# Kernel tuning notes

Measured on AMD Instinct MI355X. Metric: run time of the kernel, lower is better.

## Reference

```python
import jax, jax.numpy as jnp
import numpy as np

# photophysics rates from the original __init__
R_ISC, R_F, R_EXC, R_IC = 3e6, 5e7, 1e6, 7e7
R_ISC_S0, R_S1_OFF, R_OFF_S0 = 1e5, 2e4, 2.0e-1
RATE_MATRIX = np.array([
    [0.0,  R_EXC, 0.0,   0.0,      0.0],
    [R_F,  0.0,   R_ISC, R_S1_OFF, R_IC],
    [R_ISC_S0, 0.0, 0.0, 0.0,      0.0],
    [R_OFF_S0, 0.0, 0.0, 0.0,      0.0],
], dtype=np.float64)
ROW_SUMS = RATE_MATRIX.sum(axis=1)            # Exponential rates per state
CUM_PROBS = np.cumsum(RATE_MATRIX / ROW_SUMS[:, None], axis=1)  # (4,5) CDF rows
N_BINS = 200000      # torch.arange(0, 400, 0.002)
BIN_WIDTH = 0.002
STEPS, N_SAMPLE = 20000, 2048


def setup_inputs() -> dict:
    key = jax.random.key(0)
    k1, k2 = jax.random.split(key)
    u_cat = jax.random.uniform(k1, (STEPS, N_SAMPLE), dtype=jnp.float32)
    u_exp = jax.random.uniform(k2, (STEPS, N_SAMPLE), dtype=jnp.float32)
    return {"u_cat": u_cat, "u_exp": u_exp}


def reference(u_cat, u_exp):
    cum_probs = jnp.asarray(CUM_PROBS, dtype=jnp.float32)   # (4,5)
    row_rates = jnp.asarray(ROW_SUMS, dtype=jnp.float32)    # (4,)
    n_sample = u_cat.shape[1]

    def step(state, us):
        uc, ue = us                                  # (n,), (n,)
        cp = cum_probs[state]                        # (n,5) CDF of current state row
        # Categorical sample via inverse CDF: first bin whose cdf exceeds u
        t = jnp.argmax(uc[:, None] < cp, axis=-1)    # transition index 0..4
        photon = (t == 1)                            # photon_mat[1,0] == 1
        # Exponential dwell time in the *current* state (inverse CDF)
        dwell = -jnp.log1p(-ue) / row_rates[state]
        # transition_matrix maps t<4 -> state t, t==4 -> state 0
        new_state = jnp.where(t == 4, 0, t).astype(state.dtype)
        return new_state, (photon, dwell)

    state0 = jnp.zeros(n_sample, dtype=jnp.int32)    # all emitters start in S0
    _, (photons, dwells) = jax.lax.scan(step, state0, (u_cat, u_exp))

    cum_time = jnp.cumsum(dwells, axis=0)            # (steps, n_sample)
    bins = jnp.arange(N_BINS, dtype=jnp.float32) * BIN_WIDTH
    ind = jnp.searchsorted(bins, cum_time, side='left')  # torch.bucketize
    v = ind * photons.astype(ind.dtype)              # frame index per photon, 0 otherwise
    # on-device histogram replacing the CPU np.unique loop: counts of each v value
    hist = jnp.zeros(N_BINS + 1, dtype=jnp.int32).at[v.reshape(-1)].add(1)
    return photons.astype(jnp.float32), cum_time, hist
```

## Files before the change

### kernel.cpp

```cpp
#include <hip/hip_runtime.h>
#include <math.h>

#define STEPS  20000
#define NS     2048
#define NBINS  200000
#define SEGLEN 80
#define NSEG   250
#define NT     512000
#define NT4    128000
#define WPS    5

typedef float        f32x4 __attribute__((ext_vector_type(4)));
typedef unsigned int u32x4 __attribute__((ext_vector_type(4)));

constexpr double S1d = 5e7 + 3e6 + 2e4 + 7e7;
constexpr double P0d = 5e7 / S1d;
constexpr double P2d = 3e6 / S1d;
constexpr double P3d = 2e4 / S1d;
constexpr float C0 = (float)(P0d);
constexpr float C2 = (float)(P0d + P2d);
constexpr float C3 = (float)((P0d + P2d) + P3d);

constexpr float INV_R0 = 1.0f / 1e6f;
constexpr float INV_R1 = 1.0f / 123020000.0f;
constexpr float INV_R2 = 1.0f / 1e5f;
constexpr float INV_R3 = 5.0f;

#define WS_T1P   0u
#define WS_MAPS  10240000u
#define WS_PCNT4 10752000u
#define WS_SUMS4 12800000u
#define WS_ENTER 20992000u
#define WS_OFFS  21504000u
#define WS_PTOT  23552000u

__device__ __forceinline__ int te_decode(float u1) {
    return (u1 < C2) ? ((u1 < C0) ? 0 : 2) : ((u1 < C3) ? 3 : 0);
}
__device__ __forceinline__ int next_state(int s, int te) {
    return (s == 0) ? 1 : ((s == 1) ? te : 0);
}
__device__ __forceinline__ float inv_of(int s) {
    return (s == 0) ? INV_R0 : ((s == 1) ? INV_R1 : ((s == 2) ? INV_R2 : INV_R3));
}
__device__ __forceinline__ float dwell_base(float ue) {
    return -__logf(1.0f - ue);
}

__device__ __forceinline__ int bucketize(float v) {
    int lo = (int)(v * 500.0f) - 2;
    lo = lo < 0 ? 0 : lo;
#pragma unroll
    for (int i = 0; i < 4; ++i) lo += ((float)lo * 0.002f < v) ? 1 : 0;
    return lo > NBINS ? NBINS : lo;
}

__global__ void zero_kernel(float* __restrict__ hist, int* __restrict__ ptot) {
    int i = blockIdx.x * blockDim.x + threadIdx.x;
    if (i <= NBINS) hist[i] = 0.0f;
    if (i == 0) *ptot = 0;
}

__global__ void __launch_bounds__(256)
map_dwell_kernel(const float* __restrict__ u_cat, const float* __restrict__ u_exp,
                 unsigned int* __restrict__ t1p, unsigned char* __restrict__ maps,
                 unsigned int* __restrict__ pcnt4, float4* __restrict__ sums4)
{
    const int q = blockIdx.x * 256 + threadIdx.x;
    const int seg  = q >> 9;
    const int colq = q & 511;
    const int tbase = seg * NS + colq * 4;
    const size_t f4b = (size_t)seg * SEGLEN * (NS / 4) + colq;
    const f32x4* uc4 = (const f32x4*)u_cat + f4b;
    const f32x4* ue4 = (const f32x4*)u_exp + f4b;

    f32x4 uc[2][4], ue[2][4];
#pragma unroll
    for (int j = 0; j < 4; ++j) {
        uc[0][j] = __builtin_nontemporal_load(uc4 + (size_t)j * (NS / 4));
        ue[0][j] = ue4[(size_t)j * (NS / 4)];
    }
    int st[4][4], n[4][4];
    float s[4][4];
#pragma unroll
    for (int c = 0; c < 4; ++c)
#pragma unroll
        for (int e = 0; e < 4; ++e) { st[c][e] = e; n[c][e] = 0; s[c][e] = 0.0f; }
    unsigned int wc[4] = {0u, 0u, 0u, 0u};

#pragma unroll
    for (int ch = 0; ch < 20; ++ch) {
        const int cur = ch & 1, nxt = cur ^ 1;
        if (ch < 19) {
            const size_t rb = (size_t)(ch + 1) * 4 * (NS / 4);
#pragma unroll
            for (int j = 0; j < 4; ++j) {
                uc[nxt][j] = __builtin_nontemporal_load(uc4 + rb + (size_t)j * (NS / 4));
                ue[nxt][j] = ue4[rb + (size_t)j * (NS / 4)];
            }
        }
#pragma unroll
        for (int j = 0; j < 4; ++j) {
            const int sidx = ch * 4 + j;
#pragma unroll
            for (int c = 0; c < 4; ++c) {
                const int te = te_decode(uc[cur][j][c]);
                wc[c] |= (unsigned int)te << (2 * (sidx & 15));
                const float b = dwell_base(ue[cur][j][c]);
#pragma unroll
                for (int e = 0; e < 4; ++e) {
                    n[c][e] += (st[c][e] == 0);
                    s[c][e] += b * inv_of(st[c][e]);
                    st[c][e] = next_state(st[c][e], te);
                }
            }
        }
        if ((ch & 3) == 3) {
            u32x4 wv = {wc[0], wc[1], wc[2], wc[3]};
            *(u32x4*)(t1p + (size_t)(ch >> 2) * NT + tbase) = wv;
            wc[0] = wc[1] = wc[2] = wc[3] = 0u;
        }
    }
    unsigned int m32 = 0;
#pragma unroll
    for (int c = 0; c < 4; ++c)
        m32 |= (unsigned int)(st[c][0] | (st[c][1] << 2) | (st[c][2] << 4) | (st[c][3] << 6)) << (8 * c);
    *(unsigned int*)(maps + tbase) = m32;
    u32x4 pv;
#pragma unroll
    for (int c = 0; c < 4; ++c)
        pv[c] = (unsigned int)(n[c][0] | (n[c][1] << 8) | (n[c][2] << 16) | (n[c][3] << 24));
    *(u32x4*)(pcnt4 + tbase) = pv;
#pragma unroll
    for (int c = 0; c < 4; ++c)
        sums4[tbase + c] = make_float4(s[c][0], s[c][1], s[c][2], s[c][3]);
}

__global__ void __launch_bounds__(256)
scan_kernel(const unsigned char* __restrict__ maps, const unsigned int* __restrict__ pcnt4,
            const float4* __restrict__ sums4, unsigned char* __restrict__ enter,
            float* __restrict__ offs, int* __restrict__ ptot)
{
    const int col = blockIdx.x * 256 + threadIdx.x;
    int state = 0, P = 0;
    float off = 0.0f;

    unsigned char mpA[5], mpB[5];
    unsigned int  mtA[5], mtB[5];
    float4        s4A[5], s4B[5];
#pragma unroll
    for (int j = 0; j < 5; ++j) {
        const int idx = j * NS + col;
        mpA[j] = maps[idx]; mtA[j] = pcnt4[idx]; s4A[j] = sums4[idx];
    }
#define SCAN_PREFETCH(BUFm, BUFt, BUFs, B)                                   \
    {   const int gb = (B) * 5;                                              \
        _Pragma("unroll")                                                    \
        for (int j = 0; j < 5; ++j) {                                        \
            const int idx = (gb + j) * NS + col;                             \
            BUFm[j] = maps[idx]; BUFt[j] = pcnt4[idx]; BUFs[j] = sums4[idx]; \
        } }
#define SCAN_PROCESS(BUFm, BUFt, BUFs, B)                                    \
    {   const int gb = (B) * 5;                                              \
        _Pragma("unroll")                                                    \
        for (int j = 0; j < 5; ++j) {                                        \
            const int idx = (gb + j) * NS + col;                             \
            enter[idx] = (unsigned char)state;                               \
            offs[idx]  = off;                                                \
            const float4 s = BUFs[j];                                        \
            const float lo = (state & 1) ? s.y : s.x;                        \
            const float hi = (state & 1) ? s.w : s.z;                        \
            off += (state & 2) ? hi : lo;                                    \
            P += (int)((BUFt[j] >> (8 * state)) & 0xffu);                    \
            state = (int)((BUFm[j] >> (2 * state)) & 3u);                    \
        } }
    for (int b = 0; b < 50; b += 2) {
        SCAN_PREFETCH(mpB, mtB, s4B, b + 1)
        SCAN_PROCESS(mpA, mtA, s4A, b)
        if (b + 2 < 50) SCAN_PREFETCH(mpA, mtA, s4A, b + 2)
        SCAN_PROCESS(mpB, mtB, s4B, b + 1)
    }
#undef SCAN_PREFETCH
#undef SCAN_PROCESS

    __shared__ int red[256];
    red[threadIdx.x] = P;
    __syncthreads();
#pragma unroll
    for (int s = 128; s > 0; s >>= 1) {
        if (threadIdx.x < s) red[threadIdx.x] += red[threadIdx.x + s];
        __syncthreads();
    }
    if (threadIdx.x == 0) atomicAdd(ptot, red[0]);
}

__global__ void hist0_kernel(float* __restrict__ hist, const int* __restrict__ ptot) {
    if (threadIdx.x == 0 && blockIdx.x == 0)
        hist[0] = (float)(40960000 - *ptot);
}

__device__ __forceinline__ void wave_flush(float* __restrict__ hist, int v, float cnt) {
    unsigned long long active = __ballot(v > 0);
    while (active) {
        const int leader = __ffsll((long long)active) - 1;
        const int vl = __shfl(v, leader, 64);
        const unsigned long long match = __ballot(v == vl);
        float c = (v == vl) ? cnt : 0.0f;
#pragma unroll
        for (int o = 32; o > 0; o >>= 1) c += __shfl_xor(c, o, 64);
        if ((int)(threadIdx.x & 63) == leader) atomicAdd(hist + vl, c);
        active &= ~match;
    }
}

__global__ void __launch_bounds__(256)
final_kernel(const float* __restrict__ u_exp, const unsigned int* __restrict__ t1p,
             const unsigned char* __restrict__ enter, const float* __restrict__ offs,
             float* __restrict__ photons, float* __restrict__ cumt,
             float* __restrict__ hist)
{
    const int q = blockIdx.x * 256 + threadIdx.x;
    const int seg  = q >> 9;
    const int colq = q & 511;
    const int tbase = seg * NS + colq * 4;
    const size_t f4b = (size_t)seg * SEGLEN * (NS / 4) + colq;
    const f32x4* pe = (const f32x4*)u_exp + f4b;
    f32x4* pph = (f32x4*)photons + f4b;
    f32x4* pcm = (f32x4*)cumt + f4b;

    u32x4 w[WPS];
#pragma unroll
    for (int k = 0; k < WPS; ++k) w[k] = *(const u32x4*)(t1p + (size_t)k * NT + tbase);

    const unsigned int e4 = *(const unsigned int*)(enter + tbase);
    const f32x4 of4 = *(const f32x4*)(offs + tbase);
    int st[4];
    float cum[4];
#pragma unroll
    for (int c = 0; c < 4; ++c) { st[c] = (int)((e4 >> (8 * c)) & 3u); cum[c] = of4[c]; }

    int   v0[4] = {0, 0, 0, 0}, v1[4] = {0, 0, 0, 0};
    float r0[4] = {0, 0, 0, 0}, r1[4] = {0, 0, 0, 0};

    f32x4 ue[2][4];
#pragma unroll
    for (int j = 0; j < 4; ++j) ue[0][j] = pe[(size_t)j * (NS / 4)];

#pragma unroll
    for (int ch = 0; ch < 20; ++ch) {
        const int cur = ch & 1, nxt = cur ^ 1;
        if (ch < 19) {
            const size_t rb = (size_t)(ch + 1) * 4 * (NS / 4);
#pragma unroll
            for (int j = 0; j < 4; ++j) ue[nxt][j] = pe[rb + (size_t)j * (NS / 4)];
        }
#pragma unroll
        for (int j = 0; j < 4; ++j) {
            const int sidx = ch * 4 + j;
            f32x4 phv, cmv;
#pragma unroll
            for (int c = 0; c < 4; ++c) {
                cum[c] += dwell_base(ue[cur][j][c]) * inv_of(st[c]);
                const bool ph = (st[c] == 0);
                phv[c] = ph ? 1.0f : 0.0f;
                cmv[c] = cum[c];
                if (ph) {
                    const int v = bucketize(cum[c]);
                    if (v == v0[c])       r0[c] += 1.0f;
                    else if (v == v1[c])  r1[c] += 1.0f;
                    else if (v0[c] == 0) { v0[c] = v; r0[c] = 1.0f; }
                    else if (v1[c] == 0) { v1[c] = v; r1[c] = 1.0f; }
                    else atomicAdd(hist + v, 1.0f);
                }
                st[c] = next_state(st[c], (int)((w[sidx >> 4][c] >> (2 * (sidx & 15))) & 3u));
            }
            __builtin_nontemporal_store(phv, pph + (size_t)sidx * (NS / 4));
            __builtin_nontemporal_store(cmv, pcm + (size_t)sidx * (NS / 4));
        }
    }
#pragma unroll
    for (int c = 0; c < 4; ++c) { wave_flush(hist, v0[c], r0[c]); wave_flush(hist, v1[c], r1[c]); }
}

extern "C" void kernel_launch(void* const* d_in, const int* in_sizes, int n_in,
                              void* d_out, int out_size, void* d_ws, size_t ws_size,
                              hipStream_t stream) {
    const float* u_cat = (const float*)d_in[0];
    const float* u_exp = (const float*)d_in[1];
    float* out = (float*)d_out;
    float* photons = out;
    float* cumt    = out + (size_t)STEPS * NS;
    float* hist    = out + 2 * (size_t)STEPS * NS;

    char* ws = (char*)d_ws;
    unsigned int*  t1p   = (unsigned int*)(ws + WS_T1P);
    unsigned char* maps  = (unsigned char*)(ws + WS_MAPS);
    unsigned int*  pcnt4 = (unsigned int*)(ws + WS_PCNT4);
    float4*        sums4 = (float4*)(ws + WS_SUMS4);
    unsigned char* enter = (unsigned char*)(ws + WS_ENTER);
    float*         offs  = (float*)(ws + WS_OFFS);
    int*           ptot  = (int*)(ws + WS_PTOT);

    zero_kernel<<<(NBINS + 1 + 255) / 256, 256, 0, stream>>>(hist, ptot);
    map_dwell_kernel<<<NT4 / 256, 256, 0, stream>>>(u_cat, u_exp, t1p, maps, pcnt4, sums4);
    scan_kernel<<<NS / 256, 256, 0, stream>>>(maps, pcnt4, sums4, enter, offs, ptot);
    hist0_kernel<<<1, 64, 0, stream>>>(hist, ptot);
    final_kernel<<<NT4 / 256, 256, 0, stream>>>(u_exp, t1p, enter, offs, photons, cumt, hist);
}
```

Measured before the change: 954.8 us.

## Halve per-thread columns, derive state-3 segment map from state 2, simplify histogram run caching

Each thread now processes 2 columns instead of 4, doubling the thread count for the map and final kernels so more waves are in flight. The segment map no longer simulates start state 3 separately: it reuses the state-2 trajectory, since both states always return to state 0, and corrects only the first dwell rate. The final kernel replaces the two-slot histogram cache with a bin-boundary comparison that skips bucketize for consecutive photons in the same bin, and evicts the older run with an atomic. The cost is narrower 8-byte memory accesses and possibly more atomics when bins change often.

Result: slower. 1.239 ms (+29.8%).

```diff
diff --git a/kernel.cpp b/kernel.cpp
--- a/kernel.cpp
+++ b/kernel.cpp
@@ -7,11 +7,11 @@
 #define SEGLEN 80
 #define NSEG   250
 #define NT     512000
-#define NT4    128000
+#define NT2    256000
 #define WPS    5
 
-typedef float        f32x4 __attribute__((ext_vector_type(4)));
-typedef unsigned int u32x4 __attribute__((ext_vector_type(4)));
+typedef float        f32x2 __attribute__((ext_vector_type(2)));
+typedef unsigned int u32x2 __attribute__((ext_vector_type(2)));
 
 constexpr double S1d = 5e7 + 3e6 + 2e4 + 7e7;
 constexpr double P0d = 5e7 / S1d;
@@ -67,73 +67,73 @@
                  unsigned int* __restrict__ pcnt4, float4* __restrict__ sums4)
 {
     const int q = blockIdx.x * 256 + threadIdx.x;
-    const int seg  = q >> 9;
-    const int colq = q & 511;
-    const int tbase = seg * NS + colq * 4;
-    const size_t f4b = (size_t)seg * SEGLEN * (NS / 4) + colq;
-    const f32x4* uc4 = (const f32x4*)u_cat + f4b;
-    const f32x4* ue4 = (const f32x4*)u_exp + f4b;
-
-    f32x4 uc[2][4], ue[2][4];
-#pragma unroll
-    for (int j = 0; j < 4; ++j) {
-        uc[0][j] = __builtin_nontemporal_load(uc4 + (size_t)j * (NS / 4));
-        ue[0][j] = ue4[(size_t)j * (NS / 4)];
-    }
-    int st[4][4], n[4][4];
-    float s[4][4];
-#pragma unroll
-    for (int c = 0; c < 4; ++c)
-#pragma unroll
-        for (int e = 0; e < 4; ++e) { st[c][e] = e; n[c][e] = 0; s[c][e] = 0.0f; }
-    unsigned int wc[4] = {0u, 0u, 0u, 0u};
-
-#pragma unroll
-    for (int ch = 0; ch < 20; ++ch) {
+    const int seg  = q >> 10;
+    const int colp = q & 1023;
+    const int tbase = seg * NS + colp * 2;
+    const size_t f2b = (size_t)seg * SEGLEN * (NS / 2) + colp;
+    const f32x2* uc2 = (const f32x2*)u_cat + f2b;
+    const f32x2* ue2 = (const f32x2*)u_exp + f2b;
+
+    f32x2 uc[2][8], ue[2][8];
+#pragma unroll
+    for (int j = 0; j < 8; ++j) {
+        uc[0][j] = __builtin_nontemporal_load(uc2 + (size_t)j * (NS / 2));
+        ue[0][j] = ue2[(size_t)j * (NS / 2)];
+    }
+    int st[2][3], n[2][3];
+    float s[2][3];
+#pragma unroll
+    for (int c = 0; c < 2; ++c)
+#pragma unroll
+        for (int e = 0; e < 3; ++e) { st[c][e] = e; n[c][e] = 0; s[c][e] = 0.0f; }
+    float b0[2] = {0.0f, 0.0f};
+    unsigned int wc[2] = {0u, 0u};
+
+#pragma unroll
+    for (int ch = 0; ch < 10; ++ch) {
         const int cur = ch & 1, nxt = cur ^ 1;
-        if (ch < 19) {
-            const size_t rb = (size_t)(ch + 1) * 4 * (NS / 4);
-#pragma unroll
-            for (int j = 0; j < 4; ++j) {
-                uc[nxt][j] = __builtin_nontemporal_load(uc4 + rb + (size_t)j * (NS / 4));
-                ue[nxt][j] = ue4[rb + (size_t)j * (NS / 4)];
+        if (ch < 9) {
+            const size_t rb = (size_t)(ch + 1) * 8 * (NS / 2);
+#pragma unroll
+            for (int j = 0; j < 8; ++j) {
+                uc[nxt][j] = __builtin_nontemporal_load(uc2 + rb + (size_t)j * (NS / 2));
+                ue[nxt][j] = ue2[rb + (size_t)j * (NS / 2)];
             }
         }
 #pragma unroll
-        for (int j = 0; j < 4; ++j) {
-            const int sidx = ch * 4 + j;
-#pragma unroll
-            for (int c = 0; c < 4; ++c) {
+        for (int j = 0; j < 8; ++j) {
+            const int sidx = ch * 8 + j;
+#pragma unroll
+            for (int c = 0; c < 2; ++c) {
                 const int te = te_decode(uc[cur][j][c]);
                 wc[c] |= (unsigned int)te << (2 * (sidx & 15));
                 const float b = dwell_base(ue[cur][j][c]);
-#pragma unroll
-                for (int e = 0; e < 4; ++e) {
+                if (sidx == 0) b0[c] = b;
+#pragma unroll
+                for (int e = 0; e < 3; ++e) {
                     n[c][e] += (st[c][e] == 0);
                     s[c][e] += b * inv_of(st[c][e]);
                     st[c][e] = next_state(st[c][e], te);
                 }
             }
         }
-        if ((ch & 3) == 3) {
-            u32x4 wv = {wc[0], wc[1], wc[2], wc[3]};
-            *(u32x4*)(t1p + (size_t)(ch >> 2) * NT + tbase) = wv;
-            wc[0] = wc[1] = wc[2] = wc[3] = 0u;
-        }
-    }
-    unsigned int m32 = 0;
-#pragma unroll
-    for (int c = 0; c < 4; ++c)
-        m32 |= (unsigned int)(st[c][0] | (st[c][1] << 2) | (st[c][2] << 4) | (st[c][3] << 6)) << (8 * c);
-    *(unsigned int*)(maps + tbase) = m32;
-    u32x4 pv;
-#pragma unroll
-    for (int c = 0; c < 4; ++c)
-        pv[c] = (unsigned int)(n[c][0] | (n[c][1] << 8) | (n[c][2] << 16) | (n[c][3] << 24));
-    *(u32x4*)(pcnt4 + tbase) = pv;
-#pragma unroll
-    for (int c = 0; c < 4; ++c)
-        sums4[tbase + c] = make_float4(s[c][0], s[c][1], s[c][2], s[c][3]);
+        if (ch & 1) {
+            u32x2 wv = {wc[0], wc[1]};
+            *(u32x2*)(t1p + (size_t)(ch >> 1) * NT + tbase) = wv;
+            wc[0] = wc[1] = 0u;
+        }
+    }
+    unsigned int m16 = 0;
+    u32x2 pv;
+#pragma unroll
+    for (int c = 0; c < 2; ++c) {
+        m16 |= (unsigned int)(st[c][0] | (st[c][1] << 2) | (st[c][2] << 4) | (st[c][2] << 6)) << (8 * c);
+        pv[c] = (unsigned int)(n[c][0] | (n[c][1] << 8) | (n[c][2] << 16) | (n[c][2] << 24));
+        const float s3 = s[c][2] + b0[c] * (INV_R3 - INV_R2);
+        sums4[tbase + c] = make_float4(s[c][0], s[c][1], s[c][2], s3);
+    }
+    *(unsigned short*)(maps + tbase) = (unsigned short)m16;
+    *(u32x2*)(pcnt4 + tbase) = pv;
 }
 
 __global__ void __launch_bounds__(256)
@@ -220,66 +220,70 @@
              float* __restrict__ hist)
 {
     const int q = blockIdx.x * 256 + threadIdx.x;
-    const int seg  = q >> 9;
-    const int colq = q & 511;
-    const int tbase = seg * NS + colq * 4;
-    const size_t f4b = (size_t)seg * SEGLEN * (NS / 4) + colq;
-    const f32x4* pe = (const f32x4*)u_exp + f4b;
-    f32x4* pph = (f32x4*)photons + f4b;
-    f32x4* pcm = (f32x4*)cumt + f4b;
-
-    u32x4 w[WPS];
-#pragma unroll
-    for (int k = 0; k < WPS; ++k) w[k] = *(const u32x4*)(t1p + (size_t)k * NT + tbase);
-
-    const unsigned int e4 = *(const unsigned int*)(enter + tbase);
-    const f32x4 of4 = *(const f32x4*)(offs + tbase);
-    int st[4];
-    float cum[4];
-#pragma unroll
-    for (int c = 0; c < 4; ++c) { st[c] = (int)((e4 >> (8 * c)) & 3u); cum[c] = of4[c]; }
-
-    int   v0[4] = {0, 0, 0, 0}, v1[4] = {0, 0, 0, 0};
-    float r0[4] = {0, 0, 0, 0}, r1[4] = {0, 0, 0, 0};
-
-    f32x4 ue[2][4];
-#pragma unroll
-    for (int j = 0; j < 4; ++j) ue[0][j] = pe[(size_t)j * (NS / 4)];
-
-#pragma unroll
-    for (int ch = 0; ch < 20; ++ch) {
+    const int seg  = q >> 10;
+    const int colp = q & 1023;
+    const int tbase = seg * NS + colp * 2;
+    const size_t f2b = (size_t)seg * SEGLEN * (NS / 2) + colp;
+    const f32x2* pe = (const f32x2*)u_exp + f2b;
+    f32x2* pph = (f32x2*)photons + f2b;
+    f32x2* pcm = (f32x2*)cumt + f2b;
+
+    u32x2 w[WPS];
+#pragma unroll
+    for (int k = 0; k < WPS; ++k) w[k] = *(const u32x2*)(t1p + (size_t)k * NT + tbase);
+
+    const unsigned int e2 = *(const unsigned short*)(enter + tbase);
+    const f32x2 of2 = *(const f32x2*)(offs + tbase);
+    int st[2];
+    float cum[2];
+#pragma unroll
+    for (int c = 0; c < 2; ++c) { st[c] = (int)((e2 >> (8 * c)) & 3u); cum[c] = of2[c]; }
+
+    int   v0[2] = {0, 0}, v1[2] = {0, 0};
+    float r0[2] = {0.0f, 0.0f}, r1[2] = {0.0f, 0.0f};
+    float bnd[2] = {-1.0f, -1.0f};
+
+    f32x2 ue[2][8];
+#pragma unroll
+    for (int j = 0; j < 8; ++j) ue[0][j] = pe[(size_t)j * (NS / 2)];
+
+#pragma unroll
+    for (int ch = 0; ch < 10; ++ch) {
         const int cur = ch & 1, nxt = cur ^ 1;
-        if (ch < 19) {
-            const size_t rb = (size_t)(ch + 1) * 4 * (NS / 4);
-#pragma unroll
-            for (int j = 0; j < 4; ++j) ue[nxt][j] = pe[rb + (size_t)j * (NS / 4)];
-        }
-#pragma unroll
-        for (int j = 0; j < 4; ++j) {
-            const int sidx = ch * 4 + j;
-            f32x4 phv, cmv;
-#pragma unroll
-            for (int c = 0; c < 4; ++c) {
+        if (ch < 9) {
+            const size_t rb = (size_t)(ch + 1) * 8 * (NS / 2);
+#pragma unroll
+            for (int j = 0; j < 8; ++j) ue[nxt][j] = pe[rb + (size_t)j * (NS / 2)];
+        }
+#pragma unroll
+        for (int j = 0; j < 8; ++j) {
+            const int sidx = ch * 8 + j;
+            f32x2 phv, cmv;
+#pragma unroll
+            for (int c = 0; c < 2; ++c) {
                 cum[c] += dwell_base(ue[cur][j][c]) * inv_of(st[c]);
                 const bool ph = (st[c] == 0);
                 phv[c] = ph ? 1.0f : 0.0f;
                 cmv[c] = cum[c];
                 if (ph) {
-                    const int v = bucketize(cum[c]);
-                    if (v == v0[c])       r0[c] += 1.0f;
-                    else if (v == v1[c])  r1[c] += 1.0f;
-                    else if (v0[c] == 0) { v0[c] = v; r0[c] = 1.0f; }
-                    else if (v1[c] == 0) { v1[c] = v; r1[c] = 1.0f; }
-                    else atomicAdd(hist + v, 1.0f);
+                    if (cum[c] <= bnd[c]) {
+                        r0[c] += 1.0f;
+                    } else {
+                        const int v = bucketize(cum[c]);
+                        if (v1[c]) atomicAdd(hist + v1[c], r1[c]);
+                        v1[c] = v0[c]; r1[c] = r0[c];
+                        v0[c] = v;     r0[c] = 1.0f;
+                        bnd[c] = (float)v * 0.002f;
+                    }
                 }
                 st[c] = next_state(st[c], (int)((w[sidx >> 4][c] >> (2 * (sidx & 15))) & 3u));
             }
-            __builtin_nontemporal_store(phv, pph + (size_t)sidx * (NS / 4));
-            __builtin_nontemporal_store(cmv, pcm + (size_t)sidx * (NS / 4));
-        }
-    }
-#pragma unroll
-    for (int c = 0; c < 4; ++c) { wave_flush(hist, v0[c], r0[c]); wave_flush(hist, v1[c], r1[c]); }
+            __builtin_nontemporal_store(phv, pph + (size_t)sidx * (NS / 2));
+            __builtin_nontemporal_store(cmv, pcm + (size_t)sidx * (NS / 2));
+        }
+    }
+#pragma unroll
+    for (int c = 0; c < 2; ++c) { wave_flush(hist, v0[c], r0[c]); wave_flush(hist, v1[c], r1[c]); }
 }
 
 extern "C" void kernel_launch(void* const* d_in, const int* in_sizes, int n_in,
@@ -302,8 +306,8 @@
     int*           ptot  = (int*)(ws + WS_PTOT);
 
     zero_kernel<<<(NBINS + 1 + 255) / 256, 256, 0, stream>>>(hist, ptot);
-    map_dwell_kernel<<<NT4 / 256, 256, 0, stream>>>(u_cat, u_exp, t1p, maps, pcnt4, sums4);
+    map_dwell_kernel<<<NT2 / 256, 256, 0, stream>>>(u_cat, u_exp, t1p, maps, pcnt4, sums4);
     scan_kernel<<<NS / 256, 256, 0, stream>>>(maps, pcnt4, sums4, enter, offs, ptot);
     hist0_kernel<<<1, 64, 0, stream>>>(hist, ptot);
-    final_kernel<<<NT4 / 256, 256, 0, stream>>>(u_exp, t1p, enter, offs, photons, cumt, hist);
-}
+    final_kernel<<<NT2 / 256, 256, 0, stream>>>(u_exp, t1p, enter, offs, photons, cumt, hist);
+}
```
